# Performance work log

Measured on AMD Instinct MI355X. Metric: run time of the kernel, lower is better.

The kernel has to match this reference:

```python
import jax, jax.numpy as jnp
import numpy as np

OUT, IN = 4096, 4096
BLOCK = 32
NBLK = IN // BLOCK  # 128


def setup_inputs() -> dict:
    key = jax.random.key(0)
    k1, k2, k3 = jax.random.split(key, 3)
    x = jax.random.normal(k1, (2, 2048, IN), dtype=jnp.float32)
    # per-block scales (GGUF stores fp16 scales; small magnitude typical)
    scales = jax.random.normal(k2, (OUT, NBLK), dtype=jnp.float32) * 0.01
    # int8 codes stored as unsigned 0..255; signed value = code - 128
    codes = jax.random.randint(k3, (OUT, NBLK, BLOCK), 0, 256, dtype=jnp.int32)
    return {"x": x, "scales": scales, "codes": codes}


def dequantize_q8_0(scales, codes):
    # scales: [out, nblk], codes: [out, nblk, 32] unsigned -> signed int8 semantics
    signed = codes.astype(jnp.float32) - 128.0
    w = scales[:, :, None] * signed            # [out, nblk, 32]
    return w.reshape(OUT, IN)                   # [out, in]


def reference(x, scales, codes):
    weight = dequantize_q8_0(scales, codes)     # [out, in]
    # nn.functional.linear: y = x @ weight.T
    return jnp.einsum("bsi,oi->bso", x, weight)
```

## Files before the change

kernel.cpp:

```cpp
#include <hip/hip_runtime.h>
#include <stdint.h>


#define M_DIM 4096
#define N_DIM 4096
#define K_DIM 4096

typedef __attribute__((ext_vector_type(8))) short bf16x8;
typedef __attribute__((ext_vector_type(4))) float f32x4;

__device__ __forceinline__ unsigned short f32_to_bf16_rne(float f) {
    unsigned u = __float_as_uint(f);
    u += 0x7fffu + ((u >> 16) & 1u);
    return (unsigned short)(u >> 16);
}

__device__ __forceinline__ void load_lds16(const void* g, void* l) {
    __builtin_amdgcn_global_load_lds(
        (const __attribute__((address_space(1))) unsigned int*)g,
        (__attribute__((address_space(3))) unsigned int*)l, 16, 0, 0);
}

__global__ __launch_bounds__(256) void prologue_kernel(
        const int* __restrict__ codes, const float* __restrict__ scales,
        unsigned short* __restrict__ W,
        const float* __restrict__ x, unsigned short* __restrict__ xb) {
    const int bid = blockIdx.x;
    if (bid < 16384) {
        const int tid = bid * 256 + threadIdx.x;
        const float s = scales[tid >> 3];
        const int4 c  = ((const int4*)codes)[tid];
        union { unsigned short u[4]; uint2 v; } p;
        p.u[0] = f32_to_bf16_rne(s * (float)(c.x - 128));
        p.u[1] = f32_to_bf16_rne(s * (float)(c.y - 128));
        p.u[2] = f32_to_bf16_rne(s * (float)(c.z - 128));
        p.u[3] = f32_to_bf16_rne(s * (float)(c.w - 128));
        ((uint2*)W)[tid] = p.v;
    } else {
        const int tid = (bid - 16384) * 256 + threadIdx.x;
        const float4 f = ((const float4*)x)[tid];
        union { unsigned short u[4]; uint2 v; } p;
        p.u[0] = f32_to_bf16_rne(f.x); p.u[1] = f32_to_bf16_rne(f.y);
        p.u[2] = f32_to_bf16_rne(f.z); p.u[3] = f32_to_bf16_rne(f.w);
        ((uint2*)xb)[tid] = p.v;
    }
}

#define BAR()   asm volatile("s_barrier" ::: "memory")
#define LGKM0() asm volatile("s_waitcnt lgkmcnt(0)" ::: "memory")
#define VMC(N)  asm volatile("s_waitcnt vmcnt(" #N ")" ::: "memory")

__global__ __launch_bounds__(512, 2) void gemm_8phase(
        const unsigned short* __restrict__ A,
        const unsigned short* __restrict__ B,
        float* __restrict__ C) {
    __shared__ unsigned short sA[2][2][256 * 32];
    __shared__ unsigned short sB[2][2][256 * 32];

    const int tid  = threadIdx.x;
    const int wave = tid >> 6;
    const int lane = tid & 63;

    const int bid  = blockIdx.x;
    const int xcd  = bid & 7;
    const int slot = bid >> 3;
    const int m0 = ((xcd >> 2) * 8 + (slot >> 2)) * 256;
    const int n0 = ((xcd & 3) * 4 + (slot & 3)) * 256;

    const int srow   = lane >> 2;
    const int schunk = (lane & 3) ^ ((lane >> 3) & 3);
    const unsigned short* Ag = A + (size_t)(m0 + wave * 32 + srow) * K_DIM + schunk * 8;
    const unsigned short* Bg = B + (size_t)(n0 + wave * 32 + srow) * K_DIM + schunk * 8;
    const int ldsW = wave * 1024;

    const int frow = lane & 15;
    const int quad = lane >> 4;
    const int wm = wave >> 2;
    const int wn = wave & 3;
    const int cswz = (quad ^ ((frow >> 1) & 3)) * 8;
    const int aOff = (wm * 128 + frow) * 32 + cswz;
    const int bOff = (wn * 64 + frow) * 32 + cswz;

    f32x4 acc[8][4] = {};
    bf16x8 a[4], b[4];

#define STG_A(BUF, KH, KT) do { \
        const unsigned short* s_ = Ag + (size_t)(KT) * 64 + (KH) * 32; \
        load_lds16(s_,                       &sA[BUF][KH][ldsW]); \
        load_lds16(s_ + (size_t)16 * K_DIM,  &sA[BUF][KH][ldsW + 512]); \
    } while (0)
#define STG_B(BUF, KH, KT) do { \
        const unsigned short* s_ = Bg + (size_t)(KT) * 64 + (KH) * 32; \
        load_lds16(s_,                       &sB[BUF][KH][ldsW]); \
        load_lds16(s_ + (size_t)16 * K_DIM,  &sB[BUF][KH][ldsW + 512]); \
    } while (0)
#define RD_A4(BUF, KH, MH) do { _Pragma("unroll") \
        for (int i_ = 0; i_ < 4; ++i_) \
            a[i_] = *(const bf16x8*)&sA[BUF][KH][aOff + ((MH) * 4 + i_) * 512]; \
    } while (0)
#define RD_B4(BUF, KH) do { _Pragma("unroll") \
        for (int i_ = 0; i_ < 4; ++i_) \
            b[i_] = *(const bf16x8*)&sB[BUF][KH][bOff + i_ * 512]; \
    } while (0)
#define MM16(MH) do { _Pragma("unroll") \
        for (int i_ = 0; i_ < 4; ++i_) { _Pragma("unroll") \
            for (int n_ = 0; n_ < 4; ++n_) \
                acc[(MH) * 4 + i_][n_] = __builtin_amdgcn_mfma_f32_16x16x32_bf16( \
                    a[i_], b[n_], acc[(MH) * 4 + i_][n_], 0, 0, 0); \
        } } while (0)

#define KTILE(BUF, OBUF, T, I1, I2, I3, I4, VMF) do { \
         \
        RD_A4(BUF, 0, 0); RD_B4(BUF, 0); \
        if (I1) { STG_A(OBUF, 1, (T) + 1); } \
        BAR(); LGKM0(); __builtin_amdgcn_s_setprio(1); \
        MM16(0); \
        __builtin_amdgcn_s_setprio(0); BAR(); \
         \
        RD_A4(BUF, 0, 1); \
        if (I2) { STG_B(BUF, 0, (T) + 2); } \
        BAR(); LGKM0(); __builtin_amdgcn_s_setprio(1); \
        MM16(1); \
        __builtin_amdgcn_s_setprio(0); BAR(); \
         \
        RD_A4(BUF, 1, 0); RD_B4(BUF, 1); \
        if (I3) { STG_A(BUF, 0, (T) + 2); } \
        BAR(); LGKM0(); __builtin_amdgcn_s_setprio(1); \
        MM16(0); \
        __builtin_amdgcn_s_setprio(0); BAR(); \
         \
        RD_A4(BUF, 1, 1); \
        if (I4) { STG_B(BUF, 1, (T) + 2); } \
        BAR(); LGKM0(); __builtin_amdgcn_s_setprio(1); \
        MM16(1); \
        __builtin_amdgcn_s_setprio(0); \
        VMF; BAR(); \
    } while (0)

    STG_A(0, 0, 0); STG_B(0, 0, 0); STG_A(0, 1, 0); STG_B(0, 1, 0);
    STG_B(1, 0, 1); STG_A(1, 0, 1); STG_B(1, 1, 1);
    VMC(6); BAR();

#pragma unroll 1
    for (int t2 = 0; t2 < 31; ++t2) {
        const int t = t2 * 2;
        KTILE(0, 1, t,     1, 1, 1, 1, VMC(6));
        KTILE(1, 0, t + 1, 1, 1, 1, 1, VMC(6));
    }
    KTILE(0, 1, 62, 1, 0, 0, 0, VMC(0));
    KTILE(1, 0, 63, 0, 0, 0, 0, (void)0);

    const size_t crow0 = (size_t)(m0 + wm * 128 + quad * 4);
    const int    ccol  = n0 + wn * 64 + frow;
#pragma unroll
    for (int mt = 0; mt < 8; ++mt)
#pragma unroll
        for (int nt = 0; nt < 4; ++nt)
#pragma unroll
            for (int r = 0; r < 4; ++r)
                C[(crow0 + mt * 16 + r) * N_DIM + ccol + nt * 16] = acc[mt][nt][r];

#undef STG_A
#undef STG_B
#undef RD_A4
#undef RD_B4
#undef MM16
#undef KTILE
}

extern "C" void kernel_launch(void* const* d_in, const int* in_sizes, int n_in,
                              void* d_out, int out_size, void* d_ws, size_t ws_size,
                              hipStream_t stream) {
    const float* x      = (const float*)d_in[0];
    const float* scales = (const float*)d_in[1];
    const int*   codes  = (const int*)d_in[2];
    float* y = (float*)d_out;

    unsigned short* Wb = (unsigned short*)d_ws;
    unsigned short* xb = (unsigned short*)((char*)d_ws + (size_t)N_DIM * K_DIM * 2);

    prologue_kernel<<<32768, 256, 0, stream>>>(codes, scales, Wb, x, xb);

    gemm_8phase<<<256, 512, 0, stream>>>(xb, Wb, y);
}
```

Measured before the change: 290.2 us.

## Double-buffer LDS fragment registers to overlap reads with MFMA phases

Splits the A and B register fragments into two sets each and issues the LDS reads for the next phase before running the MFMAs of the current phase, including a cross-tile prefetch of the next tile's first fragments. The explicit lgkmcnt(0) waits are replaced by sched_barrier, leaving LDS wait insertion to the compiler, and the vmcnt waits are retuned so the next buffer is resident before the cross-tile read. The aim is to hide LDS read latency behind matrix math. In exchange it uses more VGPRs, which could cause spills under the 2-blocks-per-CU launch bound, and makes correctness depend on the vmcnt accounting being exact.

```diff
diff --git a/kernel.cpp b/kernel.cpp
--- a/kernel.cpp
+++ b/kernel.cpp
@@ -47,8 +47,8 @@
 }
 
 #define BAR()   asm volatile("s_barrier" ::: "memory")
-#define LGKM0() asm volatile("s_waitcnt lgkmcnt(0)" ::: "memory")
 #define VMC(N)  asm volatile("s_waitcnt vmcnt(" #N ")" ::: "memory")
+#define SB0()   __builtin_amdgcn_sched_barrier(0)
 
 __global__ __launch_bounds__(512, 2) void gemm_8phase(
         const unsigned short* __restrict__ A,
@@ -82,7 +82,7 @@
     const int bOff = (wn * 64 + frow) * 32 + cswz;
 
     f32x4 acc[8][4] = {};
-    bf16x8 a[4], b[4];
+    bf16x8 aX[4], aY[4], b0r[4], b1r[4];
 
 #define STG_A(BUF, KH, KT) do { \
         const unsigned short* s_ = Ag + (size_t)(KT) * 64 + (KH) * 32; \
@@ -94,61 +94,61 @@
         load_lds16(s_,                       &sB[BUF][KH][ldsW]); \
         load_lds16(s_ + (size_t)16 * K_DIM,  &sB[BUF][KH][ldsW + 512]); \
     } while (0)
-#define RD_A4(BUF, KH, MH) do { _Pragma("unroll") \
+#define RD_A4(DST, BUF, KH, MH) do { _Pragma("unroll") \
         for (int i_ = 0; i_ < 4; ++i_) \
-            a[i_] = *(const bf16x8*)&sA[BUF][KH][aOff + ((MH) * 4 + i_) * 512]; \
+            DST[i_] = *(const bf16x8*)&sA[BUF][KH][aOff + ((MH) * 4 + i_) * 512]; \
     } while (0)
-#define RD_B4(BUF, KH) do { _Pragma("unroll") \
+#define RD_B4(DST, BUF, KH) do { _Pragma("unroll") \
         for (int i_ = 0; i_ < 4; ++i_) \
-            b[i_] = *(const bf16x8*)&sB[BUF][KH][bOff + i_ * 512]; \
+            DST[i_] = *(const bf16x8*)&sB[BUF][KH][bOff + i_ * 512]; \
     } while (0)
-#define MM16(MH) do { _Pragma("unroll") \
+#define MM16(AR, BR, MH) do { _Pragma("unroll") \
         for (int i_ = 0; i_ < 4; ++i_) { _Pragma("unroll") \
             for (int n_ = 0; n_ < 4; ++n_) \
                 acc[(MH) * 4 + i_][n_] = __builtin_amdgcn_mfma_f32_16x16x32_bf16( \
-                    a[i_], b[n_], acc[(MH) * 4 + i_][n_], 0, 0, 0); \
+                    AR[i_], BR[n_], acc[(MH) * 4 + i_][n_], 0, 0, 0); \
         } } while (0)
 
-#define KTILE(BUF, OBUF, T, I1, I2, I3, I4, VMF) do { \
+#define KTILE(BUF, OBUF, T, I0, I1, I2, I3, VM2, VM3, R3) do { \
          \
-        RD_A4(BUF, 0, 0); RD_B4(BUF, 0); \
-        if (I1) { STG_A(OBUF, 1, (T) + 1); } \
-        BAR(); LGKM0(); __builtin_amdgcn_s_setprio(1); \
-        MM16(0); \
-        __builtin_amdgcn_s_setprio(0); BAR(); \
+        RD_A4(aY, BUF, 0, 1); \
+        if (I0) { STG_A(OBUF, 1, (T) + 1); } \
+        BAR(); SB0(); \
+        __builtin_amdgcn_s_setprio(1); MM16(aX, b0r, 0); __builtin_amdgcn_s_setprio(0); \
+        BAR(); \
          \
-        RD_A4(BUF, 0, 1); \
-        if (I2) { STG_B(BUF, 0, (T) + 2); } \
-        BAR(); LGKM0(); __builtin_amdgcn_s_setprio(1); \
-        MM16(1); \
-        __builtin_amdgcn_s_setprio(0); BAR(); \
+        RD_A4(aX, BUF, 1, 0); RD_B4(b1r, BUF, 1); \
+        if (I1) { STG_B(BUF, 0, (T) + 2); } \
+        BAR(); SB0(); \
+        __builtin_amdgcn_s_setprio(1); MM16(aY, b0r, 1); __builtin_amdgcn_s_setprio(0); \
+        BAR(); \
          \
-        RD_A4(BUF, 1, 0); RD_B4(BUF, 1); \
-        if (I3) { STG_A(BUF, 0, (T) + 2); } \
-        BAR(); LGKM0(); __builtin_amdgcn_s_setprio(1); \
-        MM16(0); \
-        __builtin_amdgcn_s_setprio(0); BAR(); \
+        RD_A4(aY, BUF, 1, 1); \
+        if (I2) { STG_A(BUF, 0, (T) + 2); } \
+        BAR(); SB0(); \
+        __builtin_amdgcn_s_setprio(1); MM16(aX, b1r, 0); __builtin_amdgcn_s_setprio(0); \
+        VM2; BAR(); \
          \
-        RD_A4(BUF, 1, 1); \
-        if (I4) { STG_B(BUF, 1, (T) + 2); } \
-        BAR(); LGKM0(); __builtin_amdgcn_s_setprio(1); \
-        MM16(1); \
-        __builtin_amdgcn_s_setprio(0); \
-        VMF; BAR(); \
+        if (R3) { RD_A4(aX, OBUF, 0, 0); RD_B4(b0r, OBUF, 0); } \
+        if (I3) { STG_B(BUF, 1, (T) + 2); } \
+        BAR(); SB0(); \
+        __builtin_amdgcn_s_setprio(1); MM16(aY, b1r, 1); __builtin_amdgcn_s_setprio(0); \
+        VM3; BAR(); \
     } while (0)
 
     STG_A(0, 0, 0); STG_B(0, 0, 0); STG_A(0, 1, 0); STG_B(0, 1, 0);
     STG_B(1, 0, 1); STG_A(1, 0, 1); STG_B(1, 1, 1);
     VMC(6); BAR();
+    RD_A4(aX, 0, 0, 0); RD_B4(b0r, 0, 0);
 
 #pragma unroll 1
     for (int t2 = 0; t2 < 31; ++t2) {
         const int t = t2 * 2;
-        KTILE(0, 1, t,     1, 1, 1, 1, VMC(6));
-        KTILE(1, 0, t + 1, 1, 1, 1, 1, VMC(6));
+        KTILE(0, 1, t,     1, 1, 1, 1, VMC(8), VMC(6), 1);
+        KTILE(1, 0, t + 1, 1, 1, 1, 1, VMC(8), VMC(6), 1);
     }
-    KTILE(0, 1, 62, 1, 0, 0, 0, VMC(0));
-    KTILE(1, 0, 63, 0, 0, 0, 0, (void)0);
+    KTILE(0, 1, 62, 1, 0, 0, 0, VMC(4), VMC(0), 1);
+    KTILE(1, 0, 63, 0, 0, 0, 0, (void)0, (void)0, 0);
 
     const size_t crow0 = (size_t)(m0 + wm * 128 + quad * 4);
     const int    ccol  = n0 + wn * 64 + frow;
```

Measured after the change: 288.0 us. Within noise of the previous version (-0.8%).
